# Optimization experiments

Hardware: AMD Instinct MI355X
Metric: run time of the kernel (lower is better)

Reference implementation:

```python
import jax, jax.numpy as jnp
import numpy as np

FILTER_SIZE = 8
INPUT_DIM = 128
KERNEL_SIZE = 256


def setup_inputs() -> dict:
    key = jax.random.key(0)
    k1, k2, k3, k4 = jax.random.split(key, 4)
    user_batch = jax.random.normal(k1, (32, 2048, INPUT_DIM), dtype=jnp.float32)
    # Params initialized like torch.rand (uniform [0,1))
    filt = jax.random.uniform(k2, (FILTER_SIZE, INPUT_DIM), dtype=jnp.float32)
    W_k = jax.random.uniform(k3, (FILTER_SIZE * INPUT_DIM, KERNEL_SIZE), dtype=jnp.float32)
    b_k = jax.random.uniform(k4, (KERNEL_SIZE,), dtype=jnp.float32)
    return {"user_batch": user_batch, "filt": filt, "W_k": W_k, "b_k": b_k}


def reference(user_batch, filt, W_k, b_k):
    B, L, D = user_batch.shape
    F = filt.shape[0]
    n_win = L - F  # NOTE: original loop is range(0, L - F): exactly L - F windows
    # Gather sliding windows: [B, n_win, F, D]
    idx = jnp.arange(n_win)[:, None] + jnp.arange(F)[None, :]
    windows = user_batch[:, idx, :]
    # Elementwise mul with filter then contract flattened (F*D) against W_k
    W = W_k.reshape(F, D, -1)  # [F, D, K]
    out = jnp.einsum('blfd,fd,fdk->blk', windows, filt, W)
    return jax.nn.relu(out + b_k)
```

## Files before the change

### kernel.cpp

```cpp
#include <hip/hip_runtime.h>


#define L_SZ   2048
#define NWIN   2040
#define BM     128
#define MT     16

typedef __attribute__((ext_vector_type(8)))  short bf16x8;
typedef __attribute__((ext_vector_type(4)))  short bf16x4;
typedef __attribute__((ext_vector_type(16))) float f32x16;

static __device__ __forceinline__ short f2bf(float f) {
    union { float f; unsigned u; } v; v.f = f;
    unsigned r = v.u + 0x7FFFu + ((v.u >> 16) & 1u);
    return (short)(r >> 16);
}

static __device__ __forceinline__ void gload_lds16(const short* g, short* l) {
    __builtin_amdgcn_global_load_lds(
        (const __attribute__((address_space(1))) unsigned int*)g,
        (__attribute__((address_space(3))) unsigned int*)l, 16, 0, 0);
}

__global__ __launch_bounds__(256) void prep_w_kernel(
    const float* __restrict__ Wk, const float* __restrict__ filt,
    short* __restrict__ wp2)
{
    int g   = blockIdx.x * 256 + threadIdx.x;
    int R   = g >> 10;
    int w   = g & 1023;
    int np  = w >> 2;
    int pos = w & 3;
    int cs  = pos ^ ((np >> 1) & 3);
    int kb  = R * 32 + cs * 8;
    bf16x8 o;
    #pragma unroll
    for (int jj = 0; jj < 8; ++jj)
        o[jj] = f2bf(Wk[(size_t)(kb + jj) * 256 + np] * filt[kb + jj]);
    *reinterpret_cast<bf16x8*>(&wp2[(size_t)g * 8]) = o;
}

__global__ __launch_bounds__(512, 4) void cnn_enc_kernel(
    const float* __restrict__ ub, const short* __restrict__ wp2,
    const float* __restrict__ bk, float* __restrict__ out)
{
    __shared__ short sA[135 * 136];
    __shared__ short sB[2 * 8192];

    const int tid   = threadIdx.x;
    const int bid   = blockIdx.x;
    const int mt    = bid & 15;
    const int batch = bid >> 4;
    const int l0    = mt * BM;

    const int lane = tid & 63;
    const int wave = tid >> 6;
    const int wm   = wave >> 2;
    const int wn   = wave & 3;
    const int l32  = lane & 31;
    const int half = lane >> 5;

    auto stageA = [&](int q) {
        for (int idx = tid; idx < 135 * 8; idx += 512) {
            int r  = idx >> 3;
            int c4 = idx & 7;
            int rg = l0 + r; if (rg > L_SZ - 1) rg = L_SZ - 1;
            const float4 v = *reinterpret_cast<const float4*>(
                ub + (((size_t)batch * L_SZ + rg) << 7) + q * 32 + c4 * 4);
            bf16x4 o;
            o.x = f2bf(v.x); o.y = f2bf(v.y); o.z = f2bf(v.z); o.w = f2bf(v.w);
            *reinterpret_cast<bf16x4*>(&sA[r * 136 + q * 32 + c4 * 4]) = o;
        }
    };
    auto stageB = [&](int c, int buf) {
        const short* wpb = wp2 + (size_t)c * 8192;
        #pragma unroll
        for (int r = 0; r < 2; ++r) {
            int ubase = r * 512 + wave * 64;
            gload_lds16(wpb + (ubase + lane) * 8, &sB[buf * 8192 + ubase * 8]);
        }
    };

    f32x16 acc[2][2];
    #pragma unroll
    for (int i = 0; i < 2; ++i)
        #pragma unroll
        for (int j = 0; j < 2; ++j)
            acc[i][j] = (f32x16){0.f,0.f,0.f,0.f,0.f,0.f,0.f,0.f,
                                 0.f,0.f,0.f,0.f,0.f,0.f,0.f,0.f};

    int aoff[2];
    #pragma unroll
    for (int i = 0; i < 2; ++i)
        aoff[i] = (wm * 64 + i * 32 + l32) * 136 + half * 8;
    int bnp[2], bxor[2];
    #pragma unroll
    for (int j = 0; j < 2; ++j) {
        int np = wn * 64 + j * 32 + l32;
        bnp[j]  = np * 32;
        bxor[j] = (np >> 1) & 3;
    }

    stageA(0);
    stageB(0, 0);
    __syncthreads();

    #pragma unroll 1
    for (int c = 0; c < 32; ++c) {
        if (c < 3)  stageA(c + 1);
        if (c < 31) stageB(c + 1, (c + 1) & 1);
        const int f  = c >> 2, ds = c & 3;
        const int bb = (c & 1) * 8192;
        bf16x8 a[2][2], b[2][2];
        #pragma unroll
        for (int ks = 0; ks < 2; ++ks) {
            #pragma unroll
            for (int i = 0; i < 2; ++i)
                a[ks][i] = *reinterpret_cast<const bf16x8*>(
                    &sA[aoff[i] + f * 136 + ds * 32 + ks * 16]);
            #pragma unroll
            for (int j = 0; j < 2; ++j) {
                int c8 = ks * 2 + half;
                b[ks][j] = *reinterpret_cast<const bf16x8*>(
                    &sB[bb + bnp[j] + (c8 ^ bxor[j]) * 8]);
            }
        }
        #pragma unroll
        for (int ks = 0; ks < 2; ++ks)
            #pragma unroll
            for (int i = 0; i < 2; ++i)
                #pragma unroll
                for (int j = 0; j < 2; ++j)
                    acc[i][j] = __builtin_amdgcn_mfma_f32_32x32x16_bf16(
                        a[ks][i], b[ks][j], acc[i][j], 0, 0, 0);
        __syncthreads();
    }

    #pragma unroll
    for (int j = 0; j < 2; ++j) {
        int n_glob = wn * 64 + j * 32 + l32;
        float bias = bk[n_glob];
        #pragma unroll
        for (int i = 0; i < 2; ++i) {
            #pragma unroll
            for (int r = 0; r < 16; ++r) {
                int row = (r & 3) + 8 * (r >> 2) + 4 * half;
                int l = l0 + wm * 64 + i * 32 + row;
                if (l < NWIN) {
                    float v = acc[i][j][r] + bias;
                    out[((size_t)batch * NWIN + l) * 256 + n_glob] =
                        v > 0.f ? v : 0.f;
                }
            }
        }
    }
}

extern "C" void kernel_launch(void* const* d_in, const int* in_sizes, int n_in,
                              void* d_out, int out_size, void* d_ws, size_t ws_size,
                              hipStream_t stream) {
    const float* ub   = (const float*)d_in[0];
    const float* filt = (const float*)d_in[1];
    const float* Wk   = (const float*)d_in[2];
    const float* bk   = (const float*)d_in[3];
    float* out = (float*)d_out;
    short* wp2 = (short*)d_ws;

    hipLaunchKernelGGL(prep_w_kernel, dim3(128), dim3(256), 0, stream,
                       Wk, filt, wp2);
    hipLaunchKernelGGL(cnn_enc_kernel, dim3(32 * MT), dim3(512), 0, stream,
                       ub, wp2, bk, out);
}
```

Measured before the change: 124.1 us.

## Prefetch full A tile upfront and deepen B pipeline with explicit waitcnt barriers

The input tile is now loaded in one batch of register loads, issued before the first two weight chunks go to LDS, and converted to bf16 afterwards. This replaces four staged A loads spread across the first loop iterations. The B weight stream now runs two chunks ahead, using manual vmcnt/lgkmcnt waits and raw s_barrier in place of __syncthreads, and MFMA issue is raised with s_setprio. Output stores become nontemporal. The cost is higher register pressure from nine float4 prefetch registers, plus fragile hand-written wait counts.

```diff
diff --git a/kernel.cpp b/kernel.cpp
--- a/kernel.cpp
+++ b/kernel.cpp
@@ -60,18 +60,6 @@
     const int l32  = lane & 31;
     const int half = lane >> 5;
 
-    auto stageA = [&](int q) {
-        for (int idx = tid; idx < 135 * 8; idx += 512) {
-            int r  = idx >> 3;
-            int c4 = idx & 7;
-            int rg = l0 + r; if (rg > L_SZ - 1) rg = L_SZ - 1;
-            const float4 v = *reinterpret_cast<const float4*>(
-                ub + (((size_t)batch * L_SZ + rg) << 7) + q * 32 + c4 * 4);
-            bf16x4 o;
-            o.x = f2bf(v.x); o.y = f2bf(v.y); o.z = f2bf(v.z); o.w = f2bf(v.w);
-            *reinterpret_cast<bf16x4*>(&sA[r * 136 + q * 32 + c4 * 4]) = o;
-        }
-    };
     auto stageB = [&](int c, int buf) {
         const short* wpb = wp2 + (size_t)c * 8192;
         #pragma unroll
@@ -80,6 +68,36 @@
             gload_lds16(wpb + (ubase + lane) * 8, &sB[buf * 8192 + ubase * 8]);
         }
     };
+
+    const float* ubb = ub + ((size_t)batch << 18);
+    float4 av[9];
+    #pragma unroll
+    for (int u = 0; u < 9; ++u) {
+        int idx = tid + u * 512;
+        if (u < 8 || idx < 4320) {
+            int r  = idx >> 5;
+            int c4 = idx & 31;
+            int rg = l0 + r; if (rg > L_SZ - 1) rg = L_SZ - 1;
+            av[u] = *reinterpret_cast<const float4*>(
+                ubb + ((size_t)rg << 7) + c4 * 4);
+        }
+    }
+    asm volatile("" ::: "memory");
+    stageB(0, 0);
+    stageB(1, 1);
+    asm volatile("" ::: "memory");
+    #pragma unroll
+    for (int u = 0; u < 9; ++u) {
+        int idx = tid + u * 512;
+        if (u < 8 || idx < 4320) {
+            int r  = idx >> 5;
+            int c4 = idx & 31;
+            bf16x4 o;
+            o.x = f2bf(av[u].x); o.y = f2bf(av[u].y);
+            o.z = f2bf(av[u].z); o.w = f2bf(av[u].w);
+            *reinterpret_cast<bf16x4*>(&sA[r * 136 + c4 * 4]) = o;
+        }
+    }
 
     f32x16 acc[2][2];
     #pragma unroll
@@ -101,14 +119,13 @@
         bxor[j] = (np >> 1) & 3;
     }
 
-    stageA(0);
-    stageB(0, 0);
-    __syncthreads();
+    asm volatile("s_waitcnt lgkmcnt(0)" ::: "memory");
+    asm volatile("s_waitcnt vmcnt(2)" ::: "memory");
+    __builtin_amdgcn_s_barrier();
+    asm volatile("" ::: "memory");
 
     #pragma unroll 1
     for (int c = 0; c < 32; ++c) {
-        if (c < 3)  stageA(c + 1);
-        if (c < 31) stageB(c + 1, (c + 1) & 1);
         const int f  = c >> 2, ds = c & 3;
         const int bb = (c & 1) * 8192;
         bf16x8 a[2][2], b[2][2];
@@ -125,6 +142,13 @@
                     &sB[bb + bnp[j] + (c8 ^ bxor[j]) * 8]);
             }
         }
+        if (c < 30) {
+            asm volatile("s_waitcnt lgkmcnt(0)" ::: "memory");
+            __builtin_amdgcn_s_barrier();
+            asm volatile("" ::: "memory");
+            stageB(c + 2, c & 1);
+        }
+        __builtin_amdgcn_s_setprio(1);
         #pragma unroll
         for (int ks = 0; ks < 2; ++ks)
             #pragma unroll
@@ -133,7 +157,13 @@
                 for (int j = 0; j < 2; ++j)
                     acc[i][j] = __builtin_amdgcn_mfma_f32_32x32x16_bf16(
                         a[ks][i], b[ks][j], acc[i][j], 0, 0, 0);
-        __syncthreads();
+        __builtin_amdgcn_s_setprio(0);
+        if (c < 31) {
+            if (c < 30) { asm volatile("s_waitcnt vmcnt(2)" ::: "memory"); }
+            else        { asm volatile("s_waitcnt vmcnt(0)" ::: "memory"); }
+            __builtin_amdgcn_s_barrier();
+            asm volatile("" ::: "memory");
+        }
     }
 
     #pragma unroll
@@ -148,8 +178,9 @@
                 int l = l0 + wm * 64 + i * 32 + row;
                 if (l < NWIN) {
                     float v = acc[i][j][r] + bias;
-                    out[((size_t)batch * NWIN + l) * 256 + n_glob] =
-                        v > 0.f ? v : 0.f;
+                    __builtin_nontemporal_store(
+                        v > 0.f ? v : 0.f,
+                        &out[((size_t)batch * NWIN + l) * 256 + n_glob]);
                 }
             }
         }
```

After: 124.9 us. Within noise of the previous version (+0.6%).

## Split output columns across two blocks and load whole input tile upfront

Applied to the files above, without the earlier changes.

The GEMM now splits the 256 output columns into two halves. This doubles the grid to 1024 blocks of 256 threads and halves the per-block B tile. The full 135x128 A tile is loaded into registers and converted to bf16 in LDS once before the main loop, replacing the staged per-quarter A loads. The weight prep layout changes to give a non-swizzled per-half B layout. The intent is better occupancy and load balance across CUs, at the cost of reading and converting the input tile twice (once per column half) and higher register pressure from 17 float4 temporaries.

```diff
diff --git a/kernel.cpp b/kernel.cpp
--- a/kernel.cpp
+++ b/kernel.cpp
@@ -24,62 +24,79 @@
 
 __global__ __launch_bounds__(256) void prep_w_kernel(
     const float* __restrict__ Wk, const float* __restrict__ filt,
-    short* __restrict__ wp2)
+    short* __restrict__ wp6)
 {
     int g   = blockIdx.x * 256 + threadIdx.x;
-    int R   = g >> 10;
-    int w   = g & 1023;
-    int np  = w >> 2;
-    int pos = w & 3;
-    int cs  = pos ^ ((np >> 1) & 3);
-    int kb  = R * 32 + cs * 8;
+    int c   = g >> 10;
+    int nh  = (g >> 9) & 1;
+    int c8  = (g >> 7) & 3;
+    int n   = g & 127;
+    int np  = nh * 128 + n;
+    int kb  = c * 32 + c8 * 8;
     bf16x8 o;
     #pragma unroll
     for (int jj = 0; jj < 8; ++jj)
         o[jj] = f2bf(Wk[(size_t)(kb + jj) * 256 + np] * filt[kb + jj]);
-    *reinterpret_cast<bf16x8*>(&wp2[(size_t)g * 8]) = o;
+    *reinterpret_cast<bf16x8*>(&wp6[(size_t)g * 8]) = o;
 }
 
-__global__ __launch_bounds__(512, 4) void cnn_enc_kernel(
-    const float* __restrict__ ub, const short* __restrict__ wp2,
+__global__ __launch_bounds__(256, 3) void cnn_enc_kernel(
+    const float* __restrict__ ub, const short* __restrict__ wp6,
     const float* __restrict__ bk, float* __restrict__ out)
 {
     __shared__ short sA[135 * 136];
-    __shared__ short sB[2 * 8192];
+    __shared__ short sB[2 * 4096];
 
     const int tid   = threadIdx.x;
     const int bid   = blockIdx.x;
-    const int mt    = bid & 15;
-    const int batch = bid >> 4;
+    const int nh    = bid & 1;
+    const int mt    = (bid >> 1) & 15;
+    const int batch = bid >> 5;
     const int l0    = mt * BM;
 
     const int lane = tid & 63;
     const int wave = tid >> 6;
-    const int wm   = wave >> 2;
-    const int wn   = wave & 3;
+    const int wm   = wave >> 1;
+    const int wn   = wave & 1;
     const int l32  = lane & 31;
     const int half = lane >> 5;
 
-    auto stageA = [&](int q) {
-        for (int idx = tid; idx < 135 * 8; idx += 512) {
-            int r  = idx >> 3;
-            int c4 = idx & 7;
-            int rg = l0 + r; if (rg > L_SZ - 1) rg = L_SZ - 1;
-            const float4 v = *reinterpret_cast<const float4*>(
-                ub + (((size_t)batch * L_SZ + rg) << 7) + q * 32 + c4 * 4);
-            bf16x4 o;
-            o.x = f2bf(v.x); o.y = f2bf(v.y); o.z = f2bf(v.z); o.w = f2bf(v.w);
-            *reinterpret_cast<bf16x4*>(&sA[r * 136 + q * 32 + c4 * 4]) = o;
+    auto stageB = [&](int c, int buf) {
+        const short* wpb = wp6 + ((size_t)c * 2 + nh) * 4096;
+        #pragma unroll
+        for (int r = 0; r < 2; ++r) {
+            int ubase = r * 256 + wave * 64;
+            gload_lds16(wpb + (size_t)(ubase + lane) * 8,
+                        &sB[buf * 4096 + ubase * 8]);
         }
     };
-    auto stageB = [&](int c, int buf) {
-        const short* wpb = wp2 + (size_t)c * 8192;
-        #pragma unroll
-        for (int r = 0; r < 2; ++r) {
-            int ubase = r * 512 + wave * 64;
-            gload_lds16(wpb + (ubase + lane) * 8, &sB[buf * 8192 + ubase * 8]);
+
+    const float* ubb = ub + ((size_t)batch << 18);
+    float4 av[17];
+    #pragma unroll
+    for (int u = 0; u < 17; ++u) {
+        int idx = tid + u * 256;
+        if (u < 16 || idx < 4320) {
+            int r  = idx >> 5;
+            int c4 = idx & 31;
+            int rg = l0 + r; if (rg > L_SZ - 1) rg = L_SZ - 1;
+            av[u] = *reinterpret_cast<const float4*>(
+                ubb + ((size_t)rg << 7) + c4 * 4);
         }
-    };
+    }
+    stageB(0, 0);
+    #pragma unroll
+    for (int u = 0; u < 17; ++u) {
+        int idx = tid + u * 256;
+        if (u < 16 || idx < 4320) {
+            int r  = idx >> 5;
+            int c4 = idx & 31;
+            bf16x4 o;
+            o.x = f2bf(av[u].x); o.y = f2bf(av[u].y);
+            o.z = f2bf(av[u].z); o.w = f2bf(av[u].w);
+            *reinterpret_cast<bf16x4*>(&sA[r * 136 + c4 * 4]) = o;
+        }
+    }
 
     f32x16 acc[2][2];
     #pragma unroll
@@ -93,24 +110,15 @@
     #pragma unroll
     for (int i = 0; i < 2; ++i)
         aoff[i] = (wm * 64 + i * 32 + l32) * 136 + half * 8;
-    int bnp[2], bxor[2];
-    #pragma unroll
-    for (int j = 0; j < 2; ++j) {
-        int np = wn * 64 + j * 32 + l32;
-        bnp[j]  = np * 32;
-        bxor[j] = (np >> 1) & 3;
-    }
+    const int boff = (half * 128 + wn * 64 + l32) * 8;
 
-    stageA(0);
-    stageB(0, 0);
     __syncthreads();
 
     #pragma unroll 1
     for (int c = 0; c < 32; ++c) {
-        if (c < 3)  stageA(c + 1);
         if (c < 31) stageB(c + 1, (c + 1) & 1);
         const int f  = c >> 2, ds = c & 3;
-        const int bb = (c & 1) * 8192;
+        const int bb = (c & 1) * 4096;
         bf16x8 a[2][2], b[2][2];
         #pragma unroll
         for (int ks = 0; ks < 2; ++ks) {
@@ -119,11 +127,9 @@
                 a[ks][i] = *reinterpret_cast<const bf16x8*>(
                     &sA[aoff[i] + f * 136 + ds * 32 + ks * 16]);
             #pragma unroll
-            for (int j = 0; j < 2; ++j) {
-                int c8 = ks * 2 + half;
+            for (int j = 0; j < 2; ++j)
                 b[ks][j] = *reinterpret_cast<const bf16x8*>(
-                    &sB[bb + bnp[j] + (c8 ^ bxor[j]) * 8]);
-            }
+                    &sB[bb + boff + ks * 2048 + j * 256]);
         }
         #pragma unroll
         for (int ks = 0; ks < 2; ++ks)
@@ -138,7 +144,7 @@
 
     #pragma unroll
     for (int j = 0; j < 2; ++j) {
-        int n_glob = wn * 64 + j * 32 + l32;
+        int n_glob = nh * 128 + wn * 64 + j * 32 + l32;
         float bias = bk[n_glob];
         #pragma unroll
         for (int i = 0; i < 2; ++i) {
@@ -164,10 +170,10 @@
     const float* Wk   = (const float*)d_in[2];
     const float* bk   = (const float*)d_in[3];
     float* out = (float*)d_out;
-    short* wp2 = (short*)d_ws;
+    short* wp6 = (short*)d_ws;
 
     hipLaunchKernelGGL(prep_w_kernel, dim3(128), dim3(256), 0, stream,
-                       Wk, filt, wp2);
-    hipLaunchKernelGGL(cnn_enc_kernel, dim3(32 * MT), dim3(512), 0, stream,
-                       ub, wp2, bk, out);
+                       Wk, filt, wp6);
+    hipLaunchKernelGGL(cnn_enc_kernel, dim3(32 * MT * 2), dim3(256), 0, stream,
+                       ub, wp6, bk, out);
 }
```

Result: slower. 146.5 us (+18.0%).
